# Kernel optimization log

Measured on AMD Instinct MI355X. Metric: run time of the kernel, lower is better.

Reference implementation:

```python
import jax, jax.numpy as jnp
import numpy as np
from jax import lax

EPS = 1e-5
DN = ('NCHW', 'OIHW', 'NCHW')


def setup_inputs() -> dict:
    key = jax.random.key(0)
    ks = jax.random.split(key, 16)
    B = 8192
    # uniform(0,1): every pixel nonzero => all voxels active => sparse conv == dense conv
    x = jax.random.uniform(ks[0], (B, 1, 28, 28), dtype=jnp.float32)

    def conv_params(kw, kb, c_in, c_out, k):
        scale = 1.0 / np.sqrt(c_in * k * k)
        w = jax.random.normal(kw, (c_out, c_in, k, k), dtype=jnp.float32) * scale
        b = jax.random.normal(kb, (c_out,), dtype=jnp.float32) * scale
        return w, b

    w0, b0 = conv_params(ks[1], ks[2], 1, 32, 3)
    w1, b1 = conv_params(ks[3], ks[4], 32, 64, 2)
    w2, b2 = conv_params(ks[5], ks[6], 64, 128, 2)
    # BatchNorm affine params (init: gamma=1, beta=0)
    g0, be0 = jnp.ones((32,), jnp.float32), jnp.zeros((32,), jnp.float32)
    g1, be1 = jnp.ones((64,), jnp.float32), jnp.zeros((64,), jnp.float32)
    g2, be2 = jnp.ones((128,), jnp.float32), jnp.zeros((128,), jnp.float32)
    w_fc = jax.random.normal(ks[7], (10, 128), dtype=jnp.float32) * (1.0 / np.sqrt(128))
    b_fc = jax.random.normal(ks[8], (10,), dtype=jnp.float32) * (1.0 / np.sqrt(128))
    return dict(x=x, w0=w0, b0=b0, g0=g0, be0=be0,
                w1=w1, b1=b1, g1=g1, be1=be1,
                w2=w2, b2=b2, g2=g2, be2=be2,
                w_fc=w_fc, b_fc=b_fc)


def _conv_bn_relu(x, w, b, g, be, stride, padding):
    # sparse conv on fully-active grid == dense conv
    y = lax.conv_general_dilated(x, w, (stride, stride), padding,
                                 dimension_numbers=DN)
    y = y + b[None, :, None, None]
    # BatchNorm1d over (N_active, C) == stats over batch+spatial (biased var)
    mean = jnp.mean(y, axis=(0, 2, 3))
    var = jnp.var(y, axis=(0, 2, 3))
    y = (y - mean[None, :, None, None]) * lax.rsqrt(var + EPS)[None, :, None, None]
    y = y * g[None, :, None, None] + be[None, :, None, None]
    return jax.nn.relu(y)


def reference(x, w0, b0, g0, be0, w1, b1, g1, be1, w2, b2, g2, be2, w_fc, b_fc):
    h = _conv_bn_relu(x, w0, b0, g0, be0, 1, 'SAME')    # (B,32,28,28)
    h = _conv_bn_relu(h, w1, b1, g1, be1, 2, 'VALID')   # (B,64,14,14)
    h = _conv_bn_relu(h, w2, b2, g2, be2, 2, 'VALID')   # (B,128,7,7)
    pooled = jnp.mean(h, axis=(2, 3))                    # AdaptiveAvgPool2d(1)+Flatten
    return pooled @ w_fc.T + b_fc                        # (B, n_classes)
```

## Files before the change

### kernel.cpp

```cpp
#include <hip/hip_runtime.h>
#include <hip/hip_bf16.h>

typedef __bf16 bf16x8 __attribute__((ext_vector_type(8)));
typedef float  f32x4  __attribute__((ext_vector_type(4)));

#define BSZ 8192

union BW2 { __bf16 b[2]; unsigned int u; };
union FR  { unsigned int u[4]; bf16x8 v; };

__global__ __launch_bounds__(256) void k_stats0(const float* __restrict__ x,
                                                float* __restrict__ part0,
                                                const float* __restrict__ w1,
                                                const float* __restrict__ w2,
                                                __bf16* __restrict__ w1b,
                                                __bf16* __restrict__ w2b) {
    __shared__ float sred[4 * 54];
    const int tid = threadIdx.x;
    {
        int t = blockIdx.x * 256 + tid;
        if (t < 8192) {
            int oc = t >> 7, k = t & 127, c = k & 31, d = k >> 5;
            w1b[t] = (__bf16)w1[oc * 128 + c * 4 + d];
        }
        if (t < 32768) {
            int oc = t >> 8, k = t & 255, c = k & 63, d = k >> 6;
            w2b[t] = (__bf16)w2[oc * 256 + c * 4 + d];
        }
    }
    float a[54];
#pragma unroll
    for (int i = 0; i < 54; i++) a[i] = 0.f;
    const int total = BSZ * 784;
    for (int p = blockIdx.x * 256 + tid; p < total; p += gridDim.x * 256) {
        int b = p / 784, pix = p - b * 784;
        int y = pix / 28, xx = pix - y * 28;
        const float* xb = x + (long)b * 784;
        float nv[9];
#pragma unroll
        for (int dy = 0; dy < 3; dy++) {
            int yy = y + dy - 1;
#pragma unroll
            for (int dx = 0; dx < 3; dx++) {
                int x2 = xx + dx - 1;
                nv[dy * 3 + dx] = (yy >= 0 && yy < 28 && x2 >= 0 && x2 < 28) ? xb[yy * 28 + x2] : 0.f;
            }
        }
        int idx = 0;
#pragma unroll
        for (int t2 = 0; t2 < 9; t2++) {
            float vt = nv[t2];
            a[45 + t2] += vt;
#pragma unroll
            for (int u = t2; u < 9; u++) { a[idx] += vt * nv[u]; idx++; }
        }
    }
#pragma unroll
    for (int i = 0; i < 54; i++) {
        float v = a[i];
        v += __shfl_xor(v, 1);  v += __shfl_xor(v, 2);  v += __shfl_xor(v, 4);
        v += __shfl_xor(v, 8);  v += __shfl_xor(v, 16); v += __shfl_xor(v, 32);
        a[i] = v;
    }
    const int l = tid & 63, w = tid >> 6;
    if (l == 0) {
#pragma unroll
        for (int i = 0; i < 54; i++) sred[w * 54 + i] = a[i];
    }
    __syncthreads();
    if (tid < 54)
        part0[blockIdx.x * 64 + tid] = sred[tid] + sred[54 + tid] + sred[108 + tid] + sred[162 + tid];
}

__global__ void k_fin0(const float* __restrict__ part0, const float* __restrict__ w0,
                       const float* __restrict__ g0, const float* __restrict__ be0,
                       __bf16* __restrict__ wcv) {
    __shared__ float red[4 * 54];
    int t = threadIdx.x, c = t & 63, g = t >> 6;
    if (c < 54) {
        float acc = 0.f;
        for (int i = g; i < 1008; i += 4) acc += part0[i * 64 + c];
        red[g * 54 + c] = acc;
    }
    __syncthreads();
    if (t < 54) red[t] = red[t] + red[54 + t] + red[108 + t] + red[162 + t];
    __syncthreads();
    if (t < 32) {
        float wv[9];
#pragma unroll
        for (int tap = 0; tap < 9; tap++) wv[tap] = w0[t * 9 + tap];
        float sum = 0.f, sq = 0.f;
        int idx = 0;
#pragma unroll
        for (int ta = 0; ta < 9; ta++) {
            sum = fmaf(wv[ta], red[45 + ta], sum);
#pragma unroll
            for (int u = ta; u < 9; u++) {
                float coef = (u == ta) ? 1.f : 2.f;
                sq = fmaf(coef * wv[ta] * wv[u], red[idx], sq);
                idx++;
            }
        }
        float cnt = (float)BSZ * 784.f;
        float mean = sum / cnt;
        float var = sq / cnt - mean * mean;
        float A = g0[t] * rsqrtf(var + 1e-5f);
        float bias = be0[t] - mean * A;
        __bf16 bhi = (__bf16)bias;
        float blo = bias - (float)bhi;
        int nn = t >> 1, hh = t & 1;
#pragma unroll
        for (int qq = 0; qq < 4; qq++) {
#pragma unroll
            for (int e = 0; e < 8; e++) {
                float v = 0.f;
                if (qq < 3) {
                    if (e < 6) {
                        int i = e >> 1;
                        v = (float)((__bf16)(A * wv[qq * 3 + i]));
                    } else if (e == 6) {
                        float wf = A * wv[qq * 3 + 0]; v = wf - (float)((__bf16)wf);
                    } else {
                        float wf = A * wv[qq * 3 + 1]; v = wf - (float)((__bf16)wf);
                    }
                } else {
                    if (e == 0)      { float wf = A * wv[2]; v = wf - (float)((__bf16)wf); }
                    else if (e == 1) { float wf = A * wv[5]; v = wf - (float)((__bf16)wf); }
                    else if (e == 2) { float wf = A * wv[8]; v = wf - (float)((__bf16)wf); }
                    else if (e == 4) v = (float)bhi;
                    else if (e == 5) v = blo;
                }
                wcv[hh * 512 + qq * 128 + nn * 8 + e] = (__bf16)v;
            }
        }
    }
}

struct C0S {
    bf16x8 bwM0, bwM1;
    int q, n;
    int Koff, off1, off2;
    bool q3;
};

__device__ inline void c0_init(C0S& S, const __bf16* __restrict__ wcv, int l) {
    S.q = l >> 4; S.n = l & 15; S.q3 = (S.q == 3);
    S.bwM0 = *(const bf16x8*)&wcv[S.q * 128 + S.n * 8];
    S.bwM1 = *(const bf16x8*)&wcv[512 + S.q * 128 + S.n * 8];
    S.Koff = S.q3 ? 2 : S.q * 30;
    S.off1 = S.q3 ? 30 : 1;
    S.off2 = S.q3 ? 60 : 2;
}

__device__ inline void c0_produce(const C0S& S, const unsigned* __restrict__ xs2w,
                                  __bf16* sAtw, int my, int mx, bool zpad) {
    const int b00 = 2 * my * 30 + 2 * mx + S.Koff;
#pragma unroll
    for (int t = 0; t < 4; t++) {
        const int d1 = t >> 1, d0 = t & 1;
        const unsigned* p = xs2w + b00 + d1 * 30 + d0;
        unsigned v0 = p[0], v1 = p[S.off1], v2 = p[S.off2];
        unsigned pm = __builtin_amdgcn_perm(v1, v0, 0x05040100u);
        FR A;
        A.u[0] = S.q3 ? pm : v0;
        A.u[1] = S.q3 ? (v2 & 0xffffu) : v1;
        A.u[2] = S.q3 ? 0x3F803F80u : v2;
        A.u[3] = S.q3 ? 0u : pm;
        f32x4 z = {0.f, 0.f, 0.f, 0.f};
        f32x4 ac0 = __builtin_amdgcn_mfma_f32_16x16x32_bf16(A.v, S.bwM0, z, 0, 0, 0);
        f32x4 ac1 = __builtin_amdgcn_mfma_f32_16x16x32_bf16(A.v, S.bwM1, z, 0, 0, 0);
#pragma unroll
        for (int r = 0; r < 4; r++) {
            float a0 = fmaxf(ac0[r], 0.f), a1 = fmaxf(ac1[r], 0.f);
            if (zpad) { a0 = 0.f; a1 = 0.f; }
            BW2 pk; pk.b[0] = (__bf16)a0; pk.b[1] = (__bf16)a1;
            *(unsigned*)&sAtw[(S.q * 4 + r) * 136 + t * 32 + 2 * S.n] = pk.u;
        }
    }
}

__device__ inline void stage_img(unsigned* xs2w, const float* __restrict__ x,
                                 long b, int t0, int stride) {
    for (int jj = t0; jj < 784; jj += stride) {
        int yy = jj / 28, xx2 = jj - yy * 28;
        float f = x[b * 784 + jj];
        __bf16 hi = (__bf16)f;
        __bf16 lo = (__bf16)(f - (float)hi);
        BW2 pk; pk.b[0] = hi; pk.b[1] = lo;
        xs2w[(yy + 1) * 30 + xx2 + 1] = pk.u;
    }
}

__global__ __launch_bounds__(256, 4) void k_conv01(const float* __restrict__ x,
                                                   const __bf16* __restrict__ wcv,
                                                   const __bf16* __restrict__ w1b,
                                                   __bf16* __restrict__ h1,
                                                   float* __restrict__ part1) {
    __shared__ unsigned xs2a[4][900];
    __shared__ __attribute__((aligned(16))) __bf16 sAta[4][16 * 136];
    const int tid = threadIdx.x, w = tid >> 6, l = tid & 63;
    const int q = l >> 4, n = l & 15;
    unsigned* xs2w = xs2a[w];
    __bf16* sAtw = sAta[w];
    C0S S0; c0_init(S0, wcv, l);
    bf16x8 fbv[4][4];
#pragma unroll
    for (int g = 0; g < 4; g++)
#pragma unroll
        for (int kc = 0; kc < 4; kc++)
            fbv[g][kc] = *(const bf16x8*)&w1b[(4 * n + g) * 128 + kc * 32 + q * 8];
    const long b = (long)blockIdx.x * 4 + w;
    for (int i = l; i < 900; i += 64) xs2w[i] = 0u;
    stage_img(xs2w, x, b, l, 64);
    float ssum[4] = {0.f, 0.f, 0.f, 0.f}, ssq[4] = {0.f, 0.f, 0.f, 0.f};
    __bf16* hb = h1 + b * 12544;
    for (int mt = 0; mt < 13; mt++) {
        const bool last = (mt == 12);
        int mv = (last && n >= 4) ? 195 : mt * 16 + n;
        int my = mv / 14, mx = mv - my * 14;
        c0_produce(S0, xs2w, sAtw, my, mx, last && (q != 0));
        const __bf16* sa = &sAtw[n * 136 + q * 8];
        bf16x8 fav[4];
#pragma unroll
        for (int kc = 0; kc < 4; kc++) fav[kc] = *(const bf16x8*)&sa[kc * 32];
        f32x4 a[4];
        __builtin_amdgcn_s_setprio(1);
#pragma unroll
        for (int g = 0; g < 4; g++) {
            f32x4 acc = {0.f, 0.f, 0.f, 0.f};
#pragma unroll
            for (int kc = 0; kc < 4; kc++)
                acc = __builtin_amdgcn_mfma_f32_16x16x32_bf16(fav[kc], fbv[g][kc], acc, 0, 0, 0);
            a[g] = acc;
        }
        __builtin_amdgcn_s_setprio(0);
#pragma unroll
        for (int g = 0; g < 4; g++)
#pragma unroll
            for (int r = 0; r < 4; r++) {
                ssum[g] += a[g][r];
                ssq[g] = fmaf(a[g][r], a[g][r], ssq[g]);
            }
        if ((mt < 12) | (q == 0)) {
#pragma unroll
            for (int r = 0; r < 4; r++) {
                BW2 p0, p1;
                p0.b[0] = (__bf16)a[0][r]; p0.b[1] = (__bf16)a[1][r];
                p1.b[0] = (__bf16)a[2][r]; p1.b[1] = (__bf16)a[3][r];
                uint2 u; u.x = p0.u; u.y = p1.u;
                *(uint2*)&hb[(mt * 16 + q * 4 + r) * 64 + 4 * n] = u;
            }
        }
    }
#pragma unroll
    for (int g = 0; g < 4; g++) {
        ssum[g] += __shfl_xor(ssum[g], 16); ssum[g] += __shfl_xor(ssum[g], 32);
        ssq[g]  += __shfl_xor(ssq[g], 16);  ssq[g]  += __shfl_xor(ssq[g], 32);
    }
    if (l < 16) {
#pragma unroll
        for (int g = 0; g < 4; g++) {
            part1[(long)(4 * l + g) * BSZ + b] = ssum[g];
            part1[(long)(64 + 4 * l + g) * BSZ + b] = ssq[g];
        }
    }
}

__global__ __launch_bounds__(256) void k_redfin(const float* __restrict__ part,
                                                const float* __restrict__ g,
                                                const float* __restrict__ be,
                                                float* __restrict__ abc,
                                                int C, float cnt) {
    __shared__ float s1[256], s2[256];
    const int c = blockIdx.x, tid = threadIdx.x;
    float a = 0.f, bq = 0.f;
    const float* p1 = part + (long)c * BSZ;
    const float* p2 = part + (long)(C + c) * BSZ;
    for (int i = tid; i < BSZ; i += 256) { a += p1[i]; bq += p2[i]; }
    s1[tid] = a; s2[tid] = bq;
    __syncthreads();
    for (int s = 128; s > 0; s >>= 1) {
        if (tid < s) { s1[tid] += s1[tid + s]; s2[tid] += s2[tid + s]; }
        __syncthreads();
    }
    if (tid == 0) {
        float mean = s1[0] / cnt;
        float var = s2[0] / cnt - mean * mean;
        float A = g[c] * rsqrtf(var + 1e-5f);
        abc[c] = A;
        abc[C + c] = be[c] - mean * A;
    }
}

__global__ __launch_bounds__(256) void k_conv2s(__bf16* __restrict__ h1,
                                                const __bf16* __restrict__ w2b,
                                                const float* __restrict__ abc1,
                                                float* __restrict__ part2) {
    __shared__ __attribute__((aligned(16))) __bf16 sAt[2][16 * 264];
    __shared__ __attribute__((aligned(16))) __bf16 zt[16 * 136];
    __shared__ float sbn1[128];
    const int tid = threadIdx.x;
    if (tid < 128) sbn1[tid] = abc1[tid];
    const int w = tid >> 6, l = tid & 63, q = l >> 4, n = l & 15;
    bf16x8 fbv[2][8];
#pragma unroll
    for (int ntl = 0; ntl < 2; ntl++) {
        int oc = w * 32 + 2 * n + ntl;
#pragma unroll
        for (int kc = 0; kc < 8; kc++)
            fbv[ntl][kc] = *(const bf16x8*)&w2b[oc * 256 + kc * 32 + q * 8];
    }
    __syncthreads();

    for (int img = 0; img < 4; img++) {
        const int b = blockIdx.x * 4 + img;
        __bf16* src = h1 + (long)b * 12544;
        float ssum[2] = {0.f, 0.f}, ssq[2] = {0.f, 0.f};
        for (int mt = 0; mt < 4; mt++) {
#pragma unroll
            for (int it = 0; it < 2; it++) {
                int idx = it * 256 + tid;
                int rl = idx >> 5, o = (idx & 31) * 8;
                int r = mt * 16 + rl;
                bf16x8 wv;
                if (r < 49) {
                    int d = o >> 6, c = o & 63;
                    int py = r / 7, px = r - py * 7;
                    int msrc = (2 * py + (d >> 1)) * 14 + 2 * px + (d & 1);
                    bf16x8 v = *(const bf16x8*)&src[msrc * 64 + c];
#pragma unroll
                    for (int j = 0; j < 8; j++) {
                        float f = fmaxf((float)v[j] * sbn1[c + j] + sbn1[64 + c + j], 0.f);
                        wv[j] = (__bf16)f;
                    }
                } else {
#pragma unroll
                    for (int j = 0; j < 8; j++) wv[j] = (__bf16)0.0f;
                }
                *(bf16x8*)&sAt[mt & 1][rl * 264 + o] = wv;
            }
            __syncthreads();
            bf16x8 fav[8];
#pragma unroll
            for (int kc = 0; kc < 8; kc++)
                fav[kc] = *(const bf16x8*)&sAt[mt & 1][n * 264 + kc * 32 + q * 8];
            f32x4 accA = {0.f, 0.f, 0.f, 0.f}, accB = {0.f, 0.f, 0.f, 0.f};
#pragma unroll
            for (int kc = 0; kc < 8; kc++) {
                accA = __builtin_amdgcn_mfma_f32_16x16x32_bf16(fav[kc], fbv[0][kc], accA, 0, 0, 0);
                accB = __builtin_amdgcn_mfma_f32_16x16x32_bf16(fav[kc], fbv[1][kc], accB, 0, 0, 0);
            }
#pragma unroll
            for (int rr = 0; rr < 4; rr++) {
                BW2 pk; pk.b[0] = (__bf16)accA[rr]; pk.b[1] = (__bf16)accB[rr];
                *(unsigned int*)&zt[(q * 4 + rr) * 136 + w * 32 + 2 * n] = pk.u;
                ssum[0] += accA[rr]; ssq[0] = fmaf(accA[rr], accA[rr], ssq[0]);
                ssum[1] += accB[rr]; ssq[1] = fmaf(accB[rr], accB[rr], ssq[1]);
            }
            __syncthreads();
            {
                int row = tid >> 4, o = (tid & 15) * 8;
                int m = mt * 16 + row;
                if (m < 49) {
                    bf16x8 zv = *(const bf16x8*)&zt[row * 136 + o];
                    *(bf16x8*)&src[m * 128 + o] = zv;
                }
            }
        }
#pragma unroll
        for (int ntl = 0; ntl < 2; ntl++) {
            ssum[ntl] += __shfl_xor(ssum[ntl], 16); ssum[ntl] += __shfl_xor(ssum[ntl], 32);
            ssq[ntl]  += __shfl_xor(ssq[ntl], 16);  ssq[ntl]  += __shfl_xor(ssq[ntl], 32);
        }
        if (l < 16) {
#pragma unroll
            for (int ntl = 0; ntl < 2; ntl++) {
                int oc = w * 32 + 2 * l + ntl;
                part2[(long)oc * BSZ + b] = ssum[ntl];
                part2[(long)(128 + oc) * BSZ + b] = ssq[ntl];
            }
        }
    }
}

__global__ __launch_bounds__(256) void k_final(const __bf16* __restrict__ z2,
                                               const float* __restrict__ abc2,
                                               const float* __restrict__ wfc,
                                               const float* __restrict__ bfc,
                                               float* __restrict__ out) {
    __shared__ float sbn2[256];
    __shared__ float pp[16 * 128];
    __shared__ float pooled[128];
    __shared__ float fcred[80];
    const int tid = threadIdx.x;
    sbn2[tid] = abc2[tid];
    __syncthreads();
    const int g = tid & 15, c0 = g * 8, rg = tid >> 4;
    for (int img = 0; img < 4; img++) {
        const int b = blockIdx.x * 4 + img;
        const __bf16* src = z2 + (long)b * 12544;
        float acc[8];
#pragma unroll
        for (int q = 0; q < 8; q++) acc[q] = 0.f;
        for (int rr = rg; rr < 49; rr += 16) {
            bf16x8 v = *(const bf16x8*)&src[rr * 128 + c0];
#pragma unroll
            for (int q = 0; q < 8; q++) {
                float f = fmaxf((float)v[q] * sbn2[c0 + q] + sbn2[128 + c0 + q], 0.f);
                acc[q] += f;
            }
        }
        *(f32x4*)&pp[rg * 128 + c0]     = *(f32x4*)&acc[0];
        *(f32x4*)&pp[rg * 128 + c0 + 4] = *(f32x4*)&acc[4];
        __syncthreads();
        if (tid < 128) {
            float s = 0.f;
#pragma unroll
            for (int r = 0; r < 16; r++) s += pp[r * 128 + tid];
            pooled[tid] = s * (1.f / 49.f);
        }
        __syncthreads();
        if (tid < 80) {
            int o = tid >> 3, s = tid & 7;
            float a = 0.f;
#pragma unroll
            for (int j = 0; j < 16; j++) a = fmaf(pooled[s * 16 + j], wfc[o * 128 + s * 16 + j], a);
            fcred[tid] = a;
        }
        __syncthreads();
        if (tid < 10) {
            float a = bfc[tid];
#pragma unroll
            for (int s = 0; s < 8; s++) a += fcred[tid * 8 + s];
            out[(long)b * 10 + tid] = a;
        }
    }
}

extern "C" void kernel_launch(void* const* d_in, const int* in_sizes, int n_in,
                              void* d_out, int out_size, void* d_ws, size_t ws_size,
                              hipStream_t stream) {
    const float* x   = (const float*)d_in[0];
    const float* w0  = (const float*)d_in[1];
    const float* g0  = (const float*)d_in[3];
    const float* be0 = (const float*)d_in[4];
    const float* w1  = (const float*)d_in[5];
    const float* g1  = (const float*)d_in[7];
    const float* be1 = (const float*)d_in[8];
    const float* w2  = (const float*)d_in[9];
    const float* g2  = (const float*)d_in[11];
    const float* be2 = (const float*)d_in[12];
    const float* wfc = (const float*)d_in[13];
    const float* bfc = (const float*)d_in[14];
    float* out = (float*)d_out;

    float* ws    = (float*)d_ws;
    float* part0 = ws;
    __bf16* wcv  = (__bf16*)(part0 + 1008 * 64);
    float* abc0  = part0 + 1024 * 64;
    float* part1 = abc0 + 320;
    float* abc1  = part1 + 128 * BSZ;
    float* part2 = abc1 + 128;
    float* abc2  = part2 + 256 * BSZ;
    __bf16* w1b  = (__bf16*)(abc2 + 256);
    __bf16* w2b  = w1b + 8192;
    __bf16* h1   = w2b + 32768;

    k_stats0<<<dim3(1008), dim3(256), 0, stream>>>(x, part0, w1, w2, w1b, w2b);
    k_fin0<<<dim3(1), dim3(256), 0, stream>>>(part0, w0, g0, be0, wcv);
    k_conv01<<<dim3(BSZ / 4), dim3(256), 0, stream>>>(x, wcv, w1b, h1, part1);
    k_redfin<<<dim3(64), dim3(256), 0, stream>>>(part1, g1, be1, abc1, 64, (float)(BSZ * 196));
    k_conv2s<<<dim3(BSZ / 4), dim3(256), 0, stream>>>(h1, w2b, abc1, part2);
    k_redfin<<<dim3(128), dim3(256), 0, stream>>>(part2, g2, be2, abc2, 128, (float)(BSZ * 49));
    k_final<<<dim3(BSZ / 4), dim3(256), 0, stream>>>(h1, abc2, wfc, bfc, out);
}
```

Baseline: 368.5 us.

## Software-pipeline conv2 tile loads and make final pooling+FC wave-local

The conv2 kernel is flattened into a single 16-iteration loop over (image, m-tile). The next tile's global loads are issued before the current MFMA work runs, using raw barriers and raised priority around the MFMA block. MFMA results are now written straight to global as 4-byte stores, which drops the LDS staging buffer and one barrier per tile. The final kernel gives each wavefront one image and replaces the LDS reductions and block barriers with shuffle reductions, at the cost of narrower scattered stores in conv2.

```diff
diff --git a/kernel.cpp b/kernel.cpp
--- a/kernel.cpp
+++ b/kernel.cpp
@@ -297,7 +297,6 @@
                                                 const float* __restrict__ abc1,
                                                 float* __restrict__ part2) {
     __shared__ __attribute__((aligned(16))) __bf16 sAt[2][16 * 264];
-    __shared__ __attribute__((aligned(16))) __bf16 zt[16 * 136];
     __shared__ float sbn1[128];
     const int tid = threadIdx.x;
     if (tid < 128) sbn1[tid] = abc1[tid];
@@ -310,75 +309,100 @@
         for (int kc = 0; kc < 8; kc++)
             fbv[ntl][kc] = *(const bf16x8*)&w2b[oc * 256 + kc * 32 + q * 8];
     }
+    const int rlA = tid >> 5, rlB = 8 + (tid >> 5), oo = (tid & 31) * 8;
+    const int dA = oo >> 6, cA = oo & 63;
+
+    auto issue = [&](int li, bf16x8& A0, bf16x8& A1) {
+        const int img = li >> 2, mt = li & 3;
+        const __bf16* src = h1 + ((long)blockIdx.x * 4 + img) * 12544;
+        int r0 = mt * 16 + rlA;
+        if (r0 < 49) {
+            int py = r0 / 7, px = r0 - py * 7;
+            int msrc = (2 * py + (dA >> 1)) * 14 + 2 * px + (dA & 1);
+            A0 = *(const bf16x8*)&src[msrc * 64 + cA];
+        }
+        int r1 = mt * 16 + rlB;
+        if (r1 < 49) {
+            int py = r1 / 7, px = r1 - py * 7;
+            int msrc = (2 * py + (dA >> 1)) * 14 + 2 * px + (dA & 1);
+            A1 = *(const bf16x8*)&src[msrc * 64 + cA];
+        }
+    };
+    auto put = [&](int li, bf16x8 A0, bf16x8 A1) {
+        const int mt = li & 3;
+        __bf16* sb = sAt[li & 1];
+        bf16x8 wv;
+        if (mt * 16 + rlA < 49) {
+#pragma unroll
+            for (int j = 0; j < 8; j++)
+                wv[j] = (__bf16)fmaxf((float)A0[j] * sbn1[cA + j] + sbn1[64 + cA + j], 0.f);
+        } else {
+#pragma unroll
+            for (int j = 0; j < 8; j++) wv[j] = (__bf16)0.0f;
+        }
+        *(bf16x8*)&sb[rlA * 264 + oo] = wv;
+        if (mt * 16 + rlB < 49) {
+#pragma unroll
+            for (int j = 0; j < 8; j++)
+                wv[j] = (__bf16)fmaxf((float)A1[j] * sbn1[cA + j] + sbn1[64 + cA + j], 0.f);
+        } else {
+#pragma unroll
+            for (int j = 0; j < 8; j++) wv[j] = (__bf16)0.0f;
+        }
+        *(bf16x8*)&sb[rlB * 264 + oo] = wv;
+    };
+
+    bf16x8 cur0 = {}, cur1 = {}, nxt0 = {}, nxt1 = {};
+    issue(0, cur0, cur1);
     __syncthreads();
-
-    for (int img = 0; img < 4; img++) {
-        const int b = blockIdx.x * 4 + img;
-        __bf16* src = h1 + (long)b * 12544;
-        float ssum[2] = {0.f, 0.f}, ssq[2] = {0.f, 0.f};
-        for (int mt = 0; mt < 4; mt++) {
-#pragma unroll
-            for (int it = 0; it < 2; it++) {
-                int idx = it * 256 + tid;
-                int rl = idx >> 5, o = (idx & 31) * 8;
-                int r = mt * 16 + rl;
-                bf16x8 wv;
-                if (r < 49) {
-                    int d = o >> 6, c = o & 63;
-                    int py = r / 7, px = r - py * 7;
-                    int msrc = (2 * py + (d >> 1)) * 14 + 2 * px + (d & 1);
-                    bf16x8 v = *(const bf16x8*)&src[msrc * 64 + c];
-#pragma unroll
-                    for (int j = 0; j < 8; j++) {
-                        float f = fmaxf((float)v[j] * sbn1[c + j] + sbn1[64 + c + j], 0.f);
-                        wv[j] = (__bf16)f;
-                    }
-                } else {
-#pragma unroll
-                    for (int j = 0; j < 8; j++) wv[j] = (__bf16)0.0f;
+    float ssum[2] = {0.f, 0.f}, ssq[2] = {0.f, 0.f};
+    for (int li = 0; li < 16; li++) {
+        const int img = li >> 2, mt = li & 3;
+        put(li, cur0, cur1);
+        if (li < 15) issue(li + 1, nxt0, nxt1);
+        __builtin_amdgcn_sched_barrier(0);
+        asm volatile("s_waitcnt lgkmcnt(0)" ::: "memory");
+        __builtin_amdgcn_s_barrier();
+        __builtin_amdgcn_sched_barrier(0);
+        const __bf16* sb = sAt[li & 1];
+        bf16x8 fav[8];
+#pragma unroll
+        for (int kc = 0; kc < 8; kc++)
+            fav[kc] = *(const bf16x8*)&sb[n * 264 + kc * 32 + q * 8];
+        f32x4 accA = {0.f, 0.f, 0.f, 0.f}, accB = {0.f, 0.f, 0.f, 0.f};
+        __builtin_amdgcn_s_setprio(1);
+#pragma unroll
+        for (int kc = 0; kc < 8; kc++) {
+            accA = __builtin_amdgcn_mfma_f32_16x16x32_bf16(fav[kc], fbv[0][kc], accA, 0, 0, 0);
+            accB = __builtin_amdgcn_mfma_f32_16x16x32_bf16(fav[kc], fbv[1][kc], accB, 0, 0, 0);
+        }
+        __builtin_amdgcn_s_setprio(0);
+        __bf16* src = h1 + ((long)blockIdx.x * 4 + img) * 12544;
+#pragma unroll
+        for (int rr = 0; rr < 4; rr++) {
+            int m = mt * 16 + q * 4 + rr;
+            BW2 pk; pk.b[0] = (__bf16)accA[rr]; pk.b[1] = (__bf16)accB[rr];
+            if (m < 49) *(unsigned int*)&src[m * 128 + w * 32 + 2 * n] = pk.u;
+            ssum[0] += accA[rr]; ssq[0] = fmaf(accA[rr], accA[rr], ssq[0]);
+            ssum[1] += accB[rr]; ssq[1] = fmaf(accB[rr], accB[rr], ssq[1]);
+        }
+        cur0 = nxt0; cur1 = nxt1;
+        if (mt == 3) {
+            const long b = (long)blockIdx.x * 4 + img;
+#pragma unroll
+            for (int ntl = 0; ntl < 2; ntl++) {
+                ssum[ntl] += __shfl_xor(ssum[ntl], 16); ssum[ntl] += __shfl_xor(ssum[ntl], 32);
+                ssq[ntl]  += __shfl_xor(ssq[ntl], 16);  ssq[ntl]  += __shfl_xor(ssq[ntl], 32);
+            }
+            if (l < 16) {
+#pragma unroll
+                for (int ntl = 0; ntl < 2; ntl++) {
+                    int oc = w * 32 + 2 * l + ntl;
+                    part2[(long)oc * BSZ + b] = ssum[ntl];
+                    part2[(long)(128 + oc) * BSZ + b] = ssq[ntl];
                 }
-                *(bf16x8*)&sAt[mt & 1][rl * 264 + o] = wv;
-            }
-            __syncthreads();
-            bf16x8 fav[8];
-#pragma unroll
-            for (int kc = 0; kc < 8; kc++)
-                fav[kc] = *(const bf16x8*)&sAt[mt & 1][n * 264 + kc * 32 + q * 8];
-            f32x4 accA = {0.f, 0.f, 0.f, 0.f}, accB = {0.f, 0.f, 0.f, 0.f};
-#pragma unroll
-            for (int kc = 0; kc < 8; kc++) {
-                accA = __builtin_amdgcn_mfma_f32_16x16x32_bf16(fav[kc], fbv[0][kc], accA, 0, 0, 0);
-                accB = __builtin_amdgcn_mfma_f32_16x16x32_bf16(fav[kc], fbv[1][kc], accB, 0, 0, 0);
-            }
-#pragma unroll
-            for (int rr = 0; rr < 4; rr++) {
-                BW2 pk; pk.b[0] = (__bf16)accA[rr]; pk.b[1] = (__bf16)accB[rr];
-                *(unsigned int*)&zt[(q * 4 + rr) * 136 + w * 32 + 2 * n] = pk.u;
-                ssum[0] += accA[rr]; ssq[0] = fmaf(accA[rr], accA[rr], ssq[0]);
-                ssum[1] += accB[rr]; ssq[1] = fmaf(accB[rr], accB[rr], ssq[1]);
-            }
-            __syncthreads();
-            {
-                int row = tid >> 4, o = (tid & 15) * 8;
-                int m = mt * 16 + row;
-                if (m < 49) {
-                    bf16x8 zv = *(const bf16x8*)&zt[row * 136 + o];
-                    *(bf16x8*)&src[m * 128 + o] = zv;
-                }
-            }
-        }
-#pragma unroll
-        for (int ntl = 0; ntl < 2; ntl++) {
-            ssum[ntl] += __shfl_xor(ssum[ntl], 16); ssum[ntl] += __shfl_xor(ssum[ntl], 32);
-            ssq[ntl]  += __shfl_xor(ssq[ntl], 16);  ssq[ntl]  += __shfl_xor(ssq[ntl], 32);
-        }
-        if (l < 16) {
-#pragma unroll
-            for (int ntl = 0; ntl < 2; ntl++) {
-                int oc = w * 32 + 2 * l + ntl;
-                part2[(long)oc * BSZ + b] = ssum[ntl];
-                part2[(long)(128 + oc) * BSZ + b] = ssq[ntl];
-            }
+            }
+            ssum[0] = ssum[1] = ssq[0] = ssq[1] = 0.f;
         }
     }
 }
@@ -388,52 +412,52 @@
                                                const float* __restrict__ wfc,
                                                const float* __restrict__ bfc,
                                                float* __restrict__ out) {
-    __shared__ float sbn2[256];
-    __shared__ float pp[16 * 128];
-    __shared__ float pooled[128];
-    __shared__ float fcred[80];
-    const int tid = threadIdx.x;
-    sbn2[tid] = abc2[tid];
-    __syncthreads();
-    const int g = tid & 15, c0 = g * 8, rg = tid >> 4;
-    for (int img = 0; img < 4; img++) {
-        const int b = blockIdx.x * 4 + img;
-        const __bf16* src = z2 + (long)b * 12544;
-        float acc[8];
-#pragma unroll
-        for (int q = 0; q < 8; q++) acc[q] = 0.f;
-        for (int rr = rg; rr < 49; rr += 16) {
-            bf16x8 v = *(const bf16x8*)&src[rr * 128 + c0];
-#pragma unroll
-            for (int q = 0; q < 8; q++) {
-                float f = fmaxf((float)v[q] * sbn2[c0 + q] + sbn2[128 + c0 + q], 0.f);
-                acc[q] += f;
-            }
-        }
-        *(f32x4*)&pp[rg * 128 + c0]     = *(f32x4*)&acc[0];
-        *(f32x4*)&pp[rg * 128 + c0 + 4] = *(f32x4*)&acc[4];
-        __syncthreads();
-        if (tid < 128) {
-            float s = 0.f;
-#pragma unroll
-            for (int r = 0; r < 16; r++) s += pp[r * 128 + tid];
-            pooled[tid] = s * (1.f / 49.f);
-        }
-        __syncthreads();
-        if (tid < 80) {
-            int o = tid >> 3, s = tid & 7;
-            float a = 0.f;
-#pragma unroll
-            for (int j = 0; j < 16; j++) a = fmaf(pooled[s * 16 + j], wfc[o * 128 + s * 16 + j], a);
-            fcred[tid] = a;
-        }
-        __syncthreads();
-        if (tid < 10) {
-            float a = bfc[tid];
-#pragma unroll
-            for (int s = 0; s < 8; s++) a += fcred[tid * 8 + s];
-            out[(long)b * 10 + tid] = a;
-        }
+    const int tid = threadIdx.x, w = tid >> 6, l = tid & 63;
+    const int q = l >> 4, g = l & 15;
+    const long b = (long)blockIdx.x * 4 + w;
+    const __bf16* src = z2 + b * 12544;
+    f32x4 a2lo = *(const f32x4*)&abc2[g * 8];
+    f32x4 a2hi = *(const f32x4*)&abc2[g * 8 + 4];
+    f32x4 b2lo = *(const f32x4*)&abc2[128 + g * 8];
+    f32x4 b2hi = *(const f32x4*)&abc2[128 + g * 8 + 4];
+    float acc[8];
+#pragma unroll
+    for (int j = 0; j < 8; j++) acc[j] = 0.f;
+    for (int r = q; r < 49; r += 4) {
+        bf16x8 v = *(const bf16x8*)&src[r * 128 + g * 8];
+#pragma unroll
+        for (int j = 0; j < 4; j++) {
+            acc[j]     += fmaxf((float)v[j]     * a2lo[j] + b2lo[j], 0.f);
+            acc[4 + j] += fmaxf((float)v[4 + j] * a2hi[j] + b2hi[j], 0.f);
+        }
+    }
+#pragma unroll
+    for (int j = 0; j < 8; j++) {
+        acc[j] += __shfl_xor(acc[j], 16);
+        acc[j] += __shfl_xor(acc[j], 32);
+        acc[j] *= (1.f / 49.f);
+    }
+    float p[10];
+#pragma unroll
+    for (int o = 0; o < 10; o++) {
+        f32x4 w0 = *(const f32x4*)&wfc[o * 128 + g * 8];
+        f32x4 w1 = *(const f32x4*)&wfc[o * 128 + g * 8 + 4];
+        float s = 0.f;
+#pragma unroll
+        for (int j = 0; j < 4; j++) {
+            s = fmaf(acc[j], w0[j], s);
+            s = fmaf(acc[4 + j], w1[j], s);
+        }
+        p[o] = s;
+    }
+#pragma unroll
+    for (int o = 0; o < 10; o++) {
+        p[o] += __shfl_xor(p[o], 1); p[o] += __shfl_xor(p[o], 2);
+        p[o] += __shfl_xor(p[o], 4); p[o] += __shfl_xor(p[o], 8);
+    }
+    if (l == 0) {
+#pragma unroll
+        for (int o = 0; o < 10; o++) out[b * 10 + o] = p[o] + bfc[o];
     }
 }
 
```

New measurement: 367.6 us. About the same (-0.3%).
